# Kernel optimization log

Measured on AMD Instinct MI355X. Metric: run time of the kernel, lower is better.

Reference implementation:

```python
import jax, jax.numpy as jnp
import numpy as np

B, S, E, H = 4, 2048, 2048, 16
D = E // H  # head_dim = 128


def setup_inputs() -> dict:
    key = jax.random.key(0)
    kx, kq, kk, kv = jax.random.split(key, 4)
    std = 1.0 / np.sqrt(E)
    return {
        "x": jax.random.normal(kx, (B, S, E), dtype=jnp.float32),
        "Wq": jax.random.normal(kq, (E, E), dtype=jnp.float32) * std,
        "Wk": jax.random.normal(kk, (E, E), dtype=jnp.float32) * std,
        "Wv": jax.random.normal(kv, (E, E), dtype=jnp.float32) * std,
    }


def reference(x, Wq, Wk, Wv):
    b, s, _ = x.shape
    # nn.Linear(bias=False): y = x @ W.T
    q = (x @ Wq.T).reshape(b, s, H, D).transpose(0, 2, 1, 3)  # [b,h,s,d]
    k = (x @ Wk.T).reshape(b, s, H, D).transpose(0, 2, 1, 3)
    v = (x @ Wv.T).reshape(b, s, H, D).transpose(0, 2, 1, 3)
    scale = jnp.sqrt(jnp.asarray(D, dtype=jnp.float32))
    scores = jnp.einsum("bhqd,bhkd->bhqk", q, k) / scale  # [b,h,s,s]
    causal = jnp.tril(jnp.ones((s, s), dtype=bool))
    scores = jnp.where(causal, scores, -jnp.inf)
    weights = jax.nn.softmax(scores, axis=-1)
    attn = jnp.einsum("bhqk,bhkd->bhqd", weights, v)  # [b,h,s,d]
    return attn
```

## Files before the change

### kernel.cpp

```cpp
#include <hip/hip_runtime.h>
#include <hip/hip_bf16.h>
#include <stdint.h>

#define Bdim 4
#define Sdim 2048
#define Edim 2048
#define Hdim 16
#define Ddim 128

typedef unsigned short u16;
typedef unsigned int u32;
typedef __attribute__((ext_vector_type(8))) short bf16x8;
typedef __attribute__((ext_vector_type(4))) float f32x4;
typedef __attribute__((ext_vector_type(16))) float f32x16;
typedef __attribute__((ext_vector_type(4))) unsigned short u16x4;
typedef __attribute__((ext_vector_type(2))) unsigned int u32x2;

__device__ inline u16 f2bf(float f) {
  union { float f; uint32_t u; } v; v.f = f;
  uint32_t u = v.u;
  return (u16)((u + 0x7FFFu + ((u >> 16) & 1u)) >> 16);
}

__device__ inline u32 pkbf(float lo, float hi) {
  float2 t; t.x = lo; t.y = hi;
  union { __hip_bfloat162 h2; u32 u; } cv;
  cv.h2 = __float22bfloat162_rn(t);
  return cv.u;
}

__device__ inline f32x4 mfma16(bf16x8 a, bf16x8 b, f32x4 c) {
  return __builtin_amdgcn_mfma_f32_16x16x32_bf16(a, b, c, 0, 0, 0);
}
__device__ inline f32x16 mfma32(bf16x8 a, bf16x8 b, f32x16 c) {
  return __builtin_amdgcn_mfma_f32_32x32x16_bf16(a, b, c, 0, 0, 0);
}

__device__ inline void load_lds16(const void* g, const void* l) {
  __builtin_amdgcn_global_load_lds(
      (__attribute__((address_space(1))) void*)(uintptr_t)g,
      (__attribute__((address_space(3))) void*)(uint32_t)(uintptr_t)l,
      16, 0, 0);
}

__global__ void cvt_kernel(const float* __restrict__ src, u16* __restrict__ dst,
                           int n4, float scale) {
  int i = blockIdx.x * blockDim.x + threadIdx.x;
  if (i < n4) {
    float4 f = ((const float4*)src)[i];
    u16x4 o = { f2bf(f.x * scale), f2bf(f.y * scale),
                f2bf(f.z * scale), f2bf(f.w * scale) };
    ((u16x4*)dst)[i] = o;
  }
}

template <bool TRANSV>
__global__ __launch_bounds__(512, 2)
void gemm_nt(const u16* __restrict__ A, const u16* __restrict__ Bw,
             u16* __restrict__ C, int M, int N, int K) {
  __shared__ char lds[131072];

  const int tid = threadIdx.x;
  const int lane = tid & 63;
  const int w = tid >> 6;
  const int wm = w >> 2, wn = w & 3;
  const int bm = blockIdx.x, bn = blockIdx.y;
  const int NT = K >> 5;

  const int srow_off = lane >> 2;
  const int schunk = lane & 3;

  const int l15 = lane & 15;
  const int l4 = lane >> 4;
  const int rA = wm * 128 + l15;
  const int rB = wn * 64 + l15;
  const int gA = (rA + (rA >> 2)) & 3;
  const int gB = (rB + (rB >> 2)) & 3;
  const int aoff = rA * 64 + ((l4 ^ gA) << 4);
  const int boff = rB * 64 + ((l4 ^ gB) << 4);

  const u16* Agp = A + (size_t)(bm * 256) * K;
  const u16* Bgp = Bw + (size_t)(bn * 256) * K;

  f32x4 acc[8][4];
#pragma unroll
  for (int m = 0; m < 8; ++m)
#pragma unroll
    for (int n = 0; n < 4; ++n)
      acc[m][n] = (f32x4){0.f, 0.f, 0.f, 0.f};

#define GSTAGE(tt)                                                             \
  {                                                                            \
    const int slot_ = (tt) & 3;                                                \
    char* ab_ = lds + slot_ * 16384;                                           \
    char* bb_ = lds + 65536 + slot_ * 16384;                                   \
    _Pragma("unroll")                                                          \
    for (int i_ = 0; i_ < 2; ++i_) {                                           \
      const int rbase_ = w * 32 + i_ * 16;                                     \
      const int row_ = rbase_ + srow_off;                                      \
      const int src_ = schunk ^ ((row_ + (row_ >> 2)) & 3);                    \
      load_lds16(Agp + (size_t)row_ * K + (tt) * 32 + src_ * 8,                \
                 ab_ + rbase_ * 64);                                           \
      load_lds16(Bgp + (size_t)row_ * K + (tt) * 32 + src_ * 8,                \
                 bb_ + rbase_ * 64);                                           \
    }                                                                          \
  }

  GSTAGE(0);
  GSTAGE(1);
  asm volatile("s_waitcnt vmcnt(4)" ::: "memory");
  __builtin_amdgcn_s_barrier();

  for (int t = 0; t < NT; ++t) {
    if (t + 2 < NT) GSTAGE(t + 2);

    const char* ab = lds + (t & 3) * 16384 + aoff;
    const char* bb = lds + 65536 + (t & 3) * 16384 + boff;
    bf16x8 bfr[4];
#pragma unroll
    for (int n = 0; n < 4; ++n) bfr[n] = *(const bf16x8*)(bb + n * 1024);
    __builtin_amdgcn_s_setprio(1);
#pragma unroll
    for (int m = 0; m < 8; ++m) {
      bf16x8 af = *(const bf16x8*)(ab + m * 1024);
#pragma unroll
      for (int n = 0; n < 4; ++n) acc[m][n] = mfma16(af, bfr[n], acc[m][n]);
    }
    __builtin_amdgcn_s_setprio(0);

    if (t + 2 < NT) {
      asm volatile("s_waitcnt vmcnt(4)" ::: "memory");
      __builtin_amdgcn_s_barrier();
    } else if (t + 2 == NT) {
      asm volatile("s_waitcnt vmcnt(0)" ::: "memory");
      __builtin_amdgcn_s_barrier();
    }
  }
#undef GSTAGE

  const int r0 = bm * 256 + wm * 128 + (l4 << 2);
  const int c0 = bn * 256 + wn * 64 + l15;
  if (!TRANSV) {
#pragma unroll
    for (int m = 0; m < 8; ++m)
#pragma unroll
      for (int n = 0; n < 4; ++n) {
        int r = r0 + m * 16;
        int c = c0 + n * 16;
#pragma unroll
        for (int j = 0; j < 4; ++j)
          C[(size_t)(r + j) * N + c] = f2bf(acc[m][n][j]);
      }
  } else {
#pragma unroll
    for (int m = 0; m < 8; ++m)
#pragma unroll
      for (int n = 0; n < 4; ++n) {
        int ng = c0 + n * 16;
        int h = ng >> 7, d = ng & 127;
        int mg = r0 + m * 16;
        int b = mg >> 11, s = mg & 2047;
        u16x4 pk = { f2bf(acc[m][n][0]), f2bf(acc[m][n][1]),
                     f2bf(acc[m][n][2]), f2bf(acc[m][n][3]) };
        *(u16x4*)(C + ((size_t)((b * Hdim + h) * Ddim + d)) * Sdim + s) = pk;
      }
  }
}

__global__ __launch_bounds__(256)
void attn_kernel(const u16* __restrict__ Q, const u16* __restrict__ K,
                 const u16* __restrict__ Vt, float* __restrict__ O) {
  __shared__ u16 Ks[2][64 * 128];
  __shared__ u16 Vs[2][128 * 64];

  const int tid = threadIdx.x;
  const int lane = tid & 63;
  const int w = tid >> 6;
  const int l31 = lane & 31;
  const int hi = lane >> 5;

  const int bid = blockIdx.x;
  const int bh = bid & 63;
  const int qg = 15 - (bid >> 6);
  const int q0 = qg * 128;
  const int qw0 = q0 + w * 32;
  const int b = bh >> 4, h = bh & 15;

  const u16* Qb = Q + (size_t)b * Sdim * Edim + h * Ddim;
  const u16* Kb = K + (size_t)b * Sdim * Edim + h * Ddim;
  const u16* Vb = Vt + (size_t)bh * Ddim * Sdim;

  bf16x8 qf[8];
  {
    const u16* qrow = Qb + (size_t)(qw0 + l31) * Edim + hi * 8;
#pragma unroll
    for (int c = 0; c < 8; ++c) qf[c] = *(const bf16x8*)(qrow + c * 16);
  }

  f32x16 oacc[4];
#pragma unroll
  for (int d = 0; d < 4; ++d)
#pragma unroll
    for (int i = 0; i < 16; ++i) oacc[d][i] = 0.f;
  f32x16 lacc;
#pragma unroll
  for (int i = 0; i < 16; ++i) lacc[i] = 0.f;

  const short oneb = (short)0x3F80;
  const bf16x8 ones = {oneb, oneb, oneb, oneb, oneb, oneb, oneb, oneb};

  float m2 = -1e30f;
  const int qrel = qw0 + l31;

  const int nt = 2 * qg + 2;
  const int ntw = (qw0 + 31) / 64 + 1;

  const int krow_off = (lane >> 4);
  const int kchunk = lane & 15;
  const int vrow_off = (lane >> 3);
  const int vchunk = lane & 7;

#define STAGE(bufi, tt)                                                        \
  {                                                                            \
    const int kv0s = (tt) * 64;                                                \
    _Pragma("unroll")                                                          \
    for (int i = 0; i < 4; ++i) {                                              \
      const int rbase = w * 16 + i * 4;                                        \
      const int row = rbase + krow_off;                                        \
      const int cs = kchunk ^ (row & 15);                                      \
      load_lds16(Kb + (size_t)(kv0s + row) * Edim + cs * 8,                    \
                 &Ks[bufi][rbase * 128]);                                      \
    }                                                                          \
    _Pragma("unroll")                                                          \
    for (int i = 0; i < 4; ++i) {                                              \
      const int rbase = w * 32 + i * 8;                                        \
      const int row = rbase + vrow_off;                                        \
      const int cs = vchunk ^ (row & 7);                                       \
      load_lds16(Vb + (size_t)row * Sdim + kv0s + cs * 8,                      \
                 &Vs[bufi][rbase * 64]);                                       \
    }                                                                          \
  }

  STAGE(0, 0);
  __syncthreads();

  for (int t = 0; t < nt; ++t) {
    const int cur = t & 1;
    if (t + 1 < nt) STAGE(cur ^ 1, t + 1);

    if (t < ntw) {
      const int kv0 = t * 64;

      f32x16 sc0, sc1;
#pragma unroll
      for (int i = 0; i < 16; ++i) { sc0[i] = 0.f; sc1[i] = 0.f; }
#pragma unroll
      for (int c = 0; c < 8; ++c) {
        const int ch = c * 2 + hi;
        const int r0r = l31;
        const int r1r = 32 + l31;
        bf16x8 kf0 = *(const bf16x8*)&Ks[cur][r0r * 128 + (ch ^ (r0r & 15)) * 8];
        bf16x8 kf1 = *(const bf16x8*)&Ks[cur][r1r * 128 + (ch ^ (r1r & 15)) * 8];
        sc0 = mfma32(kf0, qf[c], sc0);
        sc1 = mfma32(kf1, qf[c], sc1);
      }

      float psc[32];
      float ma = -1e30f, mb = -1e30f, mc = -1e30f, md = -1e30f;
      if (kv0 + 64 > qw0) {
#pragma unroll
        for (int r = 0; r < 16; ++r) {
          const int cr = (r & 3) + 8 * (r >> 2) + 4 * hi;
          float v0 = (kv0 + cr <= qrel) ? sc0[r] : -1e30f;
          float v1 = (kv0 + 32 + cr <= qrel) ? sc1[r] : -1e30f;
          psc[r] = v0; psc[16 + r] = v1;
          if ((r & 3) == 0) { ma = fmaxf(fmaxf(ma, v0), v1); }
          else if ((r & 3) == 1) { mb = fmaxf(fmaxf(mb, v0), v1); }
          else if ((r & 3) == 2) { mc = fmaxf(fmaxf(mc, v0), v1); }
          else { md = fmaxf(fmaxf(md, v0), v1); }
        }
      } else {
#pragma unroll
        for (int r = 0; r < 16; ++r) {
          float v0 = sc0[r];
          float v1 = sc1[r];
          psc[r] = v0; psc[16 + r] = v1;
          if ((r & 3) == 0) { ma = fmaxf(fmaxf(ma, v0), v1); }
          else if ((r & 3) == 1) { mb = fmaxf(fmaxf(mb, v0), v1); }
          else if ((r & 3) == 2) { mc = fmaxf(fmaxf(mc, v0), v1); }
          else { md = fmaxf(fmaxf(md, v0), v1); }
        }
      }
      float mt = fmaxf(fmaxf(ma, mb), fmaxf(mc, md));
      u32x2 mx = __builtin_amdgcn_permlane32_swap(
          __float_as_uint(mt), __float_as_uint(mt), false, false);
      float mo = fmaxf(__uint_as_float(mx.x), __uint_as_float(mx.y));

      if (__any(mo - m2 > 8.0f)) {
        float mnew = fmaxf(m2, mo);
        float corr = __builtin_amdgcn_exp2f(m2 - mnew);
        m2 = mnew;
        lacc[0] *= corr;
#pragma unroll
        for (int d = 0; d < 4; ++d)
#pragma unroll
          for (int i = 0; i < 16; ++i) oacc[d][i] *= corr;
      }

#pragma unroll
      for (int r = 0; r < 32; ++r)
        psc[r] = __builtin_amdgcn_exp2f(psc[r] - m2);

      u32 pk[16];
#pragma unroll
      for (int i = 0; i < 16; ++i) pk[i] = pkbf(psc[2 * i], psc[2 * i + 1]);
      bf16x8 pa[4];
#pragma unroll
      for (int t2 = 0; t2 < 2; ++t2)
#pragma unroll
        for (int q2 = 0; q2 < 2; ++q2) {
          const int base = t2 * 8 + q2 * 4;
          u32x2 r0 = __builtin_amdgcn_permlane32_swap(pk[base + 0], pk[base + 2],
                                                      false, false);
          u32x2 r1 = __builtin_amdgcn_permlane32_swap(pk[base + 1], pk[base + 3],
                                                      false, false);
          union { u32 wv[4]; bf16x8 v; } cv;
          cv.wv[0] = r0.x; cv.wv[1] = r1.x; cv.wv[2] = r0.y; cv.wv[3] = r1.y;
          pa[t2 * 2 + q2] = cv.v;
        }

#pragma unroll
      for (int dblk = 0; dblk < 4; ++dblk) {
        const int row = dblk * 32 + l31;
#pragma unroll
        for (int ks = 0; ks < 4; ++ks) {
          const int ch = ks * 2 + hi;
          bf16x8 vf = *(const bf16x8*)&Vs[cur][row * 64 + (ch ^ (row & 7)) * 8];
          oacc[dblk] = mfma32(vf, pa[ks], oacc[dblk]);
        }
      }
#pragma unroll
      for (int ks = 0; ks < 4; ++ks) lacc = mfma32(ones, pa[ks], lacc);
    }

    __syncthreads();
  }

  float inv = 1.0f / lacc[0];
  float* Ob = O + ((size_t)bh * Sdim + qw0 + l31) * Ddim + hi * 4;
#pragma unroll
  for (int dblk = 0; dblk < 4; ++dblk)
#pragma unroll
    for (int g = 0; g < 4; ++g) {
      f32x4 o4 = { oacc[dblk][4 * g] * inv, oacc[dblk][4 * g + 1] * inv,
                   oacc[dblk][4 * g + 2] * inv, oacc[dblk][4 * g + 3] * inv };
      *(f32x4*)(Ob + dblk * 32 + g * 8) = o4;
    }
}

extern "C" void kernel_launch(void* const* d_in, const int* in_sizes, int n_in,
                              void* d_out, int out_size, void* d_ws, size_t ws_size,
                              hipStream_t stream) {
  const float* x  = (const float*)d_in[0];
  const float* Wq = (const float*)d_in[1];
  const float* Wk = (const float*)d_in[2];
  const float* Wv = (const float*)d_in[3];
  float* out = (float*)d_out;
  char* ws = (char*)d_ws;

  u16* xb  = (u16*)(ws);
  u16* wqb = (u16*)(ws + 33554432ull);
  u16* wkb = (u16*)(ws + 41943040ull);
  u16* wvb = (u16*)(ws + 50331648ull);
  u16* Qb  = (u16*)(ws + 58720256ull);
  u16* Kb  = (u16*)(ws + 92274688ull);
  u16* Vt  = (u16*)(ws + 125829120ull);

  const int nX = Bdim * Sdim * Edim;
  const int nW = Edim * Edim;
  const float K1SC = 0.08838834764831845f * 1.4426950408889634f;
  cvt_kernel<<<(nX / 4 + 255) / 256, 256, 0, stream>>>(x, xb, nX / 4, 1.0f);
  cvt_kernel<<<(nW / 4 + 255) / 256, 256, 0, stream>>>(Wq, wqb, nW / 4, K1SC);
  cvt_kernel<<<(nW / 4 + 255) / 256, 256, 0, stream>>>(Wk, wkb, nW / 4, 1.0f);
  cvt_kernel<<<(nW / 4 + 255) / 256, 256, 0, stream>>>(Wv, wvb, nW / 4, 1.0f);

  dim3 g(Bdim * Sdim / 256, Edim / 256);
  gemm_nt<false><<<g, 512, 0, stream>>>(xb, wqb, Qb, Bdim * Sdim, Edim, Edim);
  gemm_nt<false><<<g, 512, 0, stream>>>(xb, wkb, Kb, Bdim * Sdim, Edim, Edim);
  gemm_nt<true ><<<g, 512, 0, stream>>>(xb, wvb, Vt, Bdim * Sdim, Edim, Edim);

  attn_kernel<<<Bdim * Hdim * (Sdim / 128), 256, 0, stream>>>(Qb, Kb, Vt, out);
}
```

Measured before the change: 374.3 us.

## Fuse QKV GEMMs into one launch and deepen attention KV pipeline with smaller tiles

The three weight conversions are merged into one kernel, and the three projection GEMMs become a single launch with a z-dimension that selects weight and output. The attention kernel moves from 64-key tiles with double buffering to 32-key tiles in a 4-slot ring with two tiles in flight. It replaces __syncthreads with explicit vmcnt waits and adds s_setprio around the MFMA sections. The diagonal mask now applies to only one 32-wide tile per wave, which trims wasted masked work. The cost is twice as many loop iterations and barriers per query block, and a reworked V swizzle that may change LDS bank behaviour.

Result: slower. 407.2 us (+8.8%).

```diff
diff --git a/kernel.cpp b/kernel.cpp
--- a/kernel.cpp
+++ b/kernel.cpp
@@ -54,11 +54,30 @@
   }
 }
 
-template <bool TRANSV>
+__global__ void cvt_w_kernel(const float* __restrict__ Wq,
+                             const float* __restrict__ Wk,
+                             const float* __restrict__ Wv,
+                             u16* __restrict__ dst, float qscale) {
+  int i = blockIdx.x * blockDim.x + threadIdx.x;
+  int seg = i >> 20;
+  int off = i & 1048575;
+  const float* src = seg == 0 ? Wq : (seg == 1 ? Wk : Wv);
+  float sc = seg == 0 ? qscale : 1.0f;
+  float4 f = ((const float4*)src)[off];
+  u16x4 o = { f2bf(f.x * sc), f2bf(f.y * sc), f2bf(f.z * sc), f2bf(f.w * sc) };
+  ((u16x4*)dst)[i] = o;
+}
+
 __global__ __launch_bounds__(512, 2)
-void gemm_nt(const u16* __restrict__ A, const u16* __restrict__ Bw,
-             u16* __restrict__ C, int M, int N, int K) {
+void gemm_qkv(const u16* __restrict__ A, const u16* __restrict__ W0,
+              const u16* __restrict__ W1, const u16* __restrict__ W2,
+              u16* __restrict__ C0, u16* __restrict__ C1, u16* __restrict__ C2,
+              int M, int N, int K) {
   __shared__ char lds[131072];
+
+  const int z = blockIdx.z;
+  const u16* Bw = z == 0 ? W0 : (z == 1 ? W1 : W2);
+  u16* C = z == 0 ? C0 : (z == 1 ? C1 : C2);
 
   const int tid = threadIdx.x;
   const int lane = tid & 63;
@@ -140,7 +159,7 @@
 
   const int r0 = bm * 256 + wm * 128 + (l4 << 2);
   const int c0 = bn * 256 + wn * 64 + l15;
-  if (!TRANSV) {
+  if (z < 2) {
 #pragma unroll
     for (int m = 0; m < 8; ++m)
 #pragma unroll
@@ -170,8 +189,8 @@
 __global__ __launch_bounds__(256)
 void attn_kernel(const u16* __restrict__ Q, const u16* __restrict__ K,
                  const u16* __restrict__ Vt, float* __restrict__ O) {
-  __shared__ u16 Ks[2][64 * 128];
-  __shared__ u16 Vs[2][128 * 64];
+  __shared__ u16 Ks[4][32 * 128];
+  __shared__ u16 Vs[4][128 * 32];
 
   const int tid = threadIdx.x;
   const int lane = tid & 63;
@@ -210,85 +229,83 @@
   const bf16x8 ones = {oneb, oneb, oneb, oneb, oneb, oneb, oneb, oneb};
 
   float m2 = -1e30f;
-  const int qrel = qw0 + l31;
-
-  const int nt = 2 * qg + 2;
-  const int ntw = (qw0 + 31) / 64 + 1;
-
-  const int krow_off = (lane >> 4);
+
+  const int nt = 4 * qg + 4;
+  const int tdiag = qw0 >> 5;
+  const int ntw = tdiag + 1;
+
+  const int krow_off = lane >> 4;
   const int kchunk = lane & 15;
-  const int vrow_off = (lane >> 3);
-  const int vchunk = lane & 7;
-
-#define STAGE(bufi, tt)                                                        \
+  const int vrow_off = lane >> 2;
+  const int vchunk = lane & 3;
+
+#define STAGE(tt)                                                              \
   {                                                                            \
-    const int kv0s = (tt) * 64;                                                \
+    const int slot_ = (tt) & 3;                                                \
+    const int kv0s = (tt) * 32;                                                \
     _Pragma("unroll")                                                          \
-    for (int i = 0; i < 4; ++i) {                                              \
-      const int rbase = w * 16 + i * 4;                                        \
+    for (int i = 0; i < 2; ++i) {                                              \
+      const int rbase = w * 8 + i * 4;                                         \
       const int row = rbase + krow_off;                                        \
       const int cs = kchunk ^ (row & 15);                                      \
       load_lds16(Kb + (size_t)(kv0s + row) * Edim + cs * 8,                    \
-                 &Ks[bufi][rbase * 128]);                                      \
+                 &Ks[slot_][rbase * 128]);                                     \
     }                                                                          \
     _Pragma("unroll")                                                          \
-    for (int i = 0; i < 4; ++i) {                                              \
-      const int rbase = w * 32 + i * 8;                                        \
+    for (int i = 0; i < 2; ++i) {                                              \
+      const int rbase = w * 32 + i * 16;                                       \
       const int row = rbase + vrow_off;                                        \
-      const int cs = vchunk ^ (row & 7);                                       \
+      const int cs = vchunk ^ ((row >> 1) & 3);                                \
       load_lds16(Vb + (size_t)row * Sdim + kv0s + cs * 8,                      \
-                 &Vs[bufi][rbase * 64]);                                       \
+                 &Vs[slot_][rbase * 32]);                                      \
     }                                                                          \
   }
 
-  STAGE(0, 0);
-  __syncthreads();
+  STAGE(0);
+  STAGE(1);
+  asm volatile("s_waitcnt vmcnt(4)" ::: "memory");
+  __builtin_amdgcn_s_barrier();
 
   for (int t = 0; t < nt; ++t) {
-    const int cur = t & 1;
-    if (t + 1 < nt) STAGE(cur ^ 1, t + 1);
+    if (t + 2 < nt) STAGE(t + 2);
 
     if (t < ntw) {
-      const int kv0 = t * 64;
-
-      f32x16 sc0, sc1;
-#pragma unroll
-      for (int i = 0; i < 16; ++i) { sc0[i] = 0.f; sc1[i] = 0.f; }
+      const int cur = t & 3;
+
+      f32x16 sc;
+#pragma unroll
+      for (int i = 0; i < 16; ++i) sc[i] = 0.f;
+      __builtin_amdgcn_s_setprio(1);
 #pragma unroll
       for (int c = 0; c < 8; ++c) {
         const int ch = c * 2 + hi;
-        const int r0r = l31;
-        const int r1r = 32 + l31;
-        bf16x8 kf0 = *(const bf16x8*)&Ks[cur][r0r * 128 + (ch ^ (r0r & 15)) * 8];
-        bf16x8 kf1 = *(const bf16x8*)&Ks[cur][r1r * 128 + (ch ^ (r1r & 15)) * 8];
-        sc0 = mfma32(kf0, qf[c], sc0);
-        sc1 = mfma32(kf1, qf[c], sc1);
-      }
-
-      float psc[32];
+        bf16x8 kf = *(const bf16x8*)&Ks[cur][l31 * 128 + ((ch ^ (l31 & 15)) * 8)];
+        sc = mfma32(kf, qf[c], sc);
+      }
+      __builtin_amdgcn_s_setprio(0);
+
+      float psc[16];
       float ma = -1e30f, mb = -1e30f, mc = -1e30f, md = -1e30f;
-      if (kv0 + 64 > qw0) {
+      if (t == tdiag) {
 #pragma unroll
         for (int r = 0; r < 16; ++r) {
           const int cr = (r & 3) + 8 * (r >> 2) + 4 * hi;
-          float v0 = (kv0 + cr <= qrel) ? sc0[r] : -1e30f;
-          float v1 = (kv0 + 32 + cr <= qrel) ? sc1[r] : -1e30f;
-          psc[r] = v0; psc[16 + r] = v1;
-          if ((r & 3) == 0) { ma = fmaxf(fmaxf(ma, v0), v1); }
-          else if ((r & 3) == 1) { mb = fmaxf(fmaxf(mb, v0), v1); }
-          else if ((r & 3) == 2) { mc = fmaxf(fmaxf(mc, v0), v1); }
-          else { md = fmaxf(fmaxf(md, v0), v1); }
+          float v = (cr <= l31) ? sc[r] : -1e30f;
+          psc[r] = v;
+          if ((r & 3) == 0) ma = fmaxf(ma, v);
+          else if ((r & 3) == 1) mb = fmaxf(mb, v);
+          else if ((r & 3) == 2) mc = fmaxf(mc, v);
+          else md = fmaxf(md, v);
         }
       } else {
 #pragma unroll
         for (int r = 0; r < 16; ++r) {
-          float v0 = sc0[r];
-          float v1 = sc1[r];
-          psc[r] = v0; psc[16 + r] = v1;
-          if ((r & 3) == 0) { ma = fmaxf(fmaxf(ma, v0), v1); }
-          else if ((r & 3) == 1) { mb = fmaxf(fmaxf(mb, v0), v1); }
-          else if ((r & 3) == 2) { mc = fmaxf(fmaxf(mc, v0), v1); }
-          else { md = fmaxf(fmaxf(md, v0), v1); }
+          float v = sc[r];
+          psc[r] = v;
+          if ((r & 3) == 0) ma = fmaxf(ma, v);
+          else if ((r & 3) == 1) mb = fmaxf(mb, v);
+          else if ((r & 3) == 2) mc = fmaxf(mc, v);
+          else md = fmaxf(md, v);
         }
       }
       float mt = fmaxf(fmaxf(ma, mb), fmaxf(mc, md));
@@ -308,43 +325,50 @@
       }
 
 #pragma unroll
-      for (int r = 0; r < 32; ++r)
+      for (int r = 0; r < 16; ++r)
         psc[r] = __builtin_amdgcn_exp2f(psc[r] - m2);
 
-      u32 pk[16];
-#pragma unroll
-      for (int i = 0; i < 16; ++i) pk[i] = pkbf(psc[2 * i], psc[2 * i + 1]);
-      bf16x8 pa[4];
-#pragma unroll
-      for (int t2 = 0; t2 < 2; ++t2)
-#pragma unroll
-        for (int q2 = 0; q2 < 2; ++q2) {
-          const int base = t2 * 8 + q2 * 4;
-          u32x2 r0 = __builtin_amdgcn_permlane32_swap(pk[base + 0], pk[base + 2],
-                                                      false, false);
-          u32x2 r1 = __builtin_amdgcn_permlane32_swap(pk[base + 1], pk[base + 3],
-                                                      false, false);
-          union { u32 wv[4]; bf16x8 v; } cv;
-          cv.wv[0] = r0.x; cv.wv[1] = r1.x; cv.wv[2] = r0.y; cv.wv[3] = r1.y;
-          pa[t2 * 2 + q2] = cv.v;
-        }
-
+      u32 pk[8];
+#pragma unroll
+      for (int i = 0; i < 8; ++i) pk[i] = pkbf(psc[2 * i], psc[2 * i + 1]);
+      bf16x8 pa[2];
+#pragma unroll
+      for (int q2 = 0; q2 < 2; ++q2) {
+        const int base = q2 * 4;
+        u32x2 r0 = __builtin_amdgcn_permlane32_swap(pk[base + 0], pk[base + 2],
+                                                    false, false);
+        u32x2 r1 = __builtin_amdgcn_permlane32_swap(pk[base + 1], pk[base + 3],
+                                                    false, false);
+        union { u32 wv[4]; bf16x8 v; } cv;
+        cv.wv[0] = r0.x; cv.wv[1] = r1.x; cv.wv[2] = r0.y; cv.wv[3] = r1.y;
+        pa[q2] = cv.v;
+      }
+
+      __builtin_amdgcn_s_setprio(1);
 #pragma unroll
       for (int dblk = 0; dblk < 4; ++dblk) {
         const int row = dblk * 32 + l31;
 #pragma unroll
-        for (int ks = 0; ks < 4; ++ks) {
+        for (int ks = 0; ks < 2; ++ks) {
           const int ch = ks * 2 + hi;
-          bf16x8 vf = *(const bf16x8*)&Vs[cur][row * 64 + (ch ^ (row & 7)) * 8];
+          bf16x8 vf = *(const bf16x8*)&Vs[cur][row * 32 + ((ch ^ ((row >> 1) & 3)) * 8)];
           oacc[dblk] = mfma32(vf, pa[ks], oacc[dblk]);
         }
       }
 #pragma unroll
-      for (int ks = 0; ks < 4; ++ks) lacc = mfma32(ones, pa[ks], lacc);
+      for (int ks = 0; ks < 2; ++ks) lacc = mfma32(ones, pa[ks], lacc);
+      __builtin_amdgcn_s_setprio(0);
     }
 
-    __syncthreads();
-  }
+    if (t + 2 < nt) {
+      asm volatile("s_waitcnt vmcnt(4)" ::: "memory");
+      __builtin_amdgcn_s_barrier();
+    } else {
+      asm volatile("s_waitcnt vmcnt(0)" ::: "memory");
+      __builtin_amdgcn_s_barrier();
+    }
+  }
+#undef STAGE
 
   float inv = 1.0f / lacc[0];
   float* Ob = O + ((size_t)bh * Sdim + qw0 + l31) * Ddim + hi * 4;
@@ -380,14 +404,11 @@
   const int nW = Edim * Edim;
   const float K1SC = 0.08838834764831845f * 1.4426950408889634f;
   cvt_kernel<<<(nX / 4 + 255) / 256, 256, 0, stream>>>(x, xb, nX / 4, 1.0f);
-  cvt_kernel<<<(nW / 4 + 255) / 256, 256, 0, stream>>>(Wq, wqb, nW / 4, K1SC);
-  cvt_kernel<<<(nW / 4 + 255) / 256, 256, 0, stream>>>(Wk, wkb, nW / 4, 1.0f);
-  cvt_kernel<<<(nW / 4 + 255) / 256, 256, 0, stream>>>(Wv, wvb, nW / 4, 1.0f);
-
-  dim3 g(Bdim * Sdim / 256, Edim / 256);
-  gemm_nt<false><<<g, 512, 0, stream>>>(xb, wqb, Qb, Bdim * Sdim, Edim, Edim);
-  gemm_nt<false><<<g, 512, 0, stream>>>(xb, wkb, Kb, Bdim * Sdim, Edim, Edim);
-  gemm_nt<true ><<<g, 512, 0, stream>>>(xb, wvb, Vt, Bdim * Sdim, Edim, Edim);
+  cvt_w_kernel<<<(3 * nW / 4 + 255) / 256, 256, 0, stream>>>(Wq, Wk, Wv, wqb, K1SC);
+
+  dim3 g(Bdim * Sdim / 256, Edim / 256, 3);
+  gemm_qkv<<<g, 512, 0, stream>>>(xb, wqb, wkb, wvb, Qb, Kb, Vt,
+                                  Bdim * Sdim, Edim, Edim);
 
   attn_kernel<<<Bdim * Hdim * (Sdim / 128), 256, 0, stream>>>(Qb, Kb, Vt, out);
 }
```

## Interleave GEMM prefetch with split MFMA phases, add setprio in attention, fuse weight casts

Applied to the files above, without the earlier changes.

The GEMM main loop now runs in two halves. It prefetches the A tile before the first half of the MFMAs and the B tile before the second half, with extra barriers between the phases, so global-to-LDS loads spread out across compute. The attention kernel raises wave priority around its MFMA blocks. The three weight-conversion launches are merged into one kernel that writes the contiguous wq/wk/wv buffers. The extra barriers per iteration add synchronisation cost in exchange for better overlap.

After: 388.4 us. 1.04x slower.

```diff
diff --git a/kernel.cpp b/kernel.cpp
--- a/kernel.cpp
+++ b/kernel.cpp
@@ -54,6 +54,20 @@
   }
 }
 
+__global__ void cvt_w_kernel(const float* __restrict__ Wq,
+                             const float* __restrict__ Wk,
+                             const float* __restrict__ Wv,
+                             u16* __restrict__ dst, float qscale) {
+  int i = blockIdx.x * blockDim.x + threadIdx.x;
+  int seg = i >> 20;
+  int off = i & 1048575;
+  const float* src = seg == 0 ? Wq : (seg == 1 ? Wk : Wv);
+  float sc = seg == 0 ? qscale : 1.0f;
+  float4 f = ((const float4*)src)[off];
+  u16x4 o = { f2bf(f.x * sc), f2bf(f.y * sc), f2bf(f.z * sc), f2bf(f.w * sc) };
+  ((u16x4*)dst)[i] = o;
+}
+
 template <bool TRANSV>
 __global__ __launch_bounds__(512, 2)
 void gemm_nt(const u16* __restrict__ A, const u16* __restrict__ Bw,
@@ -89,11 +103,9 @@
     for (int n = 0; n < 4; ++n)
       acc[m][n] = (f32x4){0.f, 0.f, 0.f, 0.f};
 
-#define GSTAGE(tt)                                                             \
+#define GSTAGE_A(tt)                                                           \
   {                                                                            \
-    const int slot_ = (tt) & 3;                                                \
-    char* ab_ = lds + slot_ * 16384;                                           \
-    char* bb_ = lds + 65536 + slot_ * 16384;                                   \
+    char* ab_ = lds + ((tt) & 3) * 16384;                                      \
     _Pragma("unroll")                                                          \
     for (int i_ = 0; i_ < 2; ++i_) {                                           \
       const int rbase_ = w * 32 + i_ * 16;                                     \
@@ -101,42 +113,66 @@
       const int src_ = schunk ^ ((row_ + (row_ >> 2)) & 3);                    \
       load_lds16(Agp + (size_t)row_ * K + (tt) * 32 + src_ * 8,                \
                  ab_ + rbase_ * 64);                                           \
+    }                                                                          \
+  }
+#define GSTAGE_B(tt)                                                           \
+  {                                                                            \
+    char* bb_ = lds + 65536 + ((tt) & 3) * 16384;                              \
+    _Pragma("unroll")                                                          \
+    for (int i_ = 0; i_ < 2; ++i_) {                                           \
+      const int rbase_ = w * 32 + i_ * 16;                                     \
+      const int row_ = rbase_ + srow_off;                                      \
+      const int src_ = schunk ^ ((row_ + (row_ >> 2)) & 3);                    \
       load_lds16(Bgp + (size_t)row_ * K + (tt) * 32 + src_ * 8,                \
                  bb_ + rbase_ * 64);                                           \
     }                                                                          \
   }
 
-  GSTAGE(0);
-  GSTAGE(1);
+  GSTAGE_A(0); GSTAGE_B(0);
+  GSTAGE_A(1); GSTAGE_B(1);
   asm volatile("s_waitcnt vmcnt(4)" ::: "memory");
   __builtin_amdgcn_s_barrier();
 
   for (int t = 0; t < NT; ++t) {
-    if (t + 2 < NT) GSTAGE(t + 2);
-
     const char* ab = lds + (t & 3) * 16384 + aoff;
     const char* bb = lds + 65536 + (t & 3) * 16384 + boff;
-    bf16x8 bfr[4];
+    const bool pf = (t + 2 < NT);
+
+    bf16x8 bfr[4], afr[4];
 #pragma unroll
     for (int n = 0; n < 4; ++n) bfr[n] = *(const bf16x8*)(bb + n * 1024);
+#pragma unroll
+    for (int m = 0; m < 4; ++m) afr[m] = *(const bf16x8*)(ab + m * 1024);
+    if (pf) GSTAGE_A(t + 2);
+    __builtin_amdgcn_s_barrier();
     __builtin_amdgcn_s_setprio(1);
 #pragma unroll
-    for (int m = 0; m < 8; ++m) {
-      bf16x8 af = *(const bf16x8*)(ab + m * 1024);
-#pragma unroll
-      for (int n = 0; n < 4; ++n) acc[m][n] = mfma16(af, bfr[n], acc[m][n]);
+    for (int m = 0; m < 4; ++m)
+#pragma unroll
+      for (int n = 0; n < 4; ++n) acc[m][n] = mfma16(afr[m], bfr[n], acc[m][n]);
+    __builtin_amdgcn_s_setprio(0);
+    __builtin_amdgcn_s_barrier();
+
+#pragma unroll
+    for (int m = 0; m < 4; ++m) afr[m] = *(const bf16x8*)(ab + (m + 4) * 1024);
+    if (pf) GSTAGE_B(t + 2);
+    __builtin_amdgcn_s_barrier();
+    __builtin_amdgcn_s_setprio(1);
+#pragma unroll
+    for (int m = 0; m < 4; ++m)
+#pragma unroll
+      for (int n = 0; n < 4; ++n)
+        acc[m + 4][n] = mfma16(afr[m], bfr[n], acc[m + 4][n]);
+    __builtin_amdgcn_s_setprio(0);
+    if (pf) {
+      asm volatile("s_waitcnt vmcnt(4)" ::: "memory");
+    } else {
+      asm volatile("s_waitcnt vmcnt(0)" ::: "memory");
     }
-    __builtin_amdgcn_s_setprio(0);
-
-    if (t + 2 < NT) {
-      asm volatile("s_waitcnt vmcnt(4)" ::: "memory");
-      __builtin_amdgcn_s_barrier();
-    } else if (t + 2 == NT) {
-      asm volatile("s_waitcnt vmcnt(0)" ::: "memory");
-      __builtin_amdgcn_s_barrier();
-    }
-  }
-#undef GSTAGE
+    __builtin_amdgcn_s_barrier();
+  }
+#undef GSTAGE_A
+#undef GSTAGE_B
 
   const int r0 = bm * 256 + wm * 128 + (l4 << 2);
   const int c0 = bn * 256 + wn * 64 + l15;
@@ -254,6 +290,7 @@
       f32x16 sc0, sc1;
 #pragma unroll
       for (int i = 0; i < 16; ++i) { sc0[i] = 0.f; sc1[i] = 0.f; }
+      __builtin_amdgcn_s_setprio(1);
 #pragma unroll
       for (int c = 0; c < 8; ++c) {
         const int ch = c * 2 + hi;
@@ -264,6 +301,7 @@
         sc0 = mfma32(kf0, qf[c], sc0);
         sc1 = mfma32(kf1, qf[c], sc1);
       }
+      __builtin_amdgcn_s_setprio(0);
 
       float psc[32];
       float ma = -1e30f, mb = -1e30f, mc = -1e30f, md = -1e30f;
@@ -329,6 +367,7 @@
           pa[t2 * 2 + q2] = cv.v;
         }
 
+      __builtin_amdgcn_s_setprio(1);
 #pragma unroll
       for (int dblk = 0; dblk < 4; ++dblk) {
         const int row = dblk * 32 + l31;
@@ -341,10 +380,12 @@
       }
 #pragma unroll
       for (int ks = 0; ks < 4; ++ks) lacc = mfma32(ones, pa[ks], lacc);
+      __builtin_amdgcn_s_setprio(0);
     }
 
     __syncthreads();
   }
+#undef STAGE
 
   float inv = 1.0f / lacc[0];
   float* Ob = O + ((size_t)bh * Sdim + qw0 + l31) * Ddim + hi * 4;
@@ -380,9 +421,7 @@
   const int nW = Edim * Edim;
   const float K1SC = 0.08838834764831845f * 1.4426950408889634f;
   cvt_kernel<<<(nX / 4 + 255) / 256, 256, 0, stream>>>(x, xb, nX / 4, 1.0f);
-  cvt_kernel<<<(nW / 4 + 255) / 256, 256, 0, stream>>>(Wq, wqb, nW / 4, K1SC);
-  cvt_kernel<<<(nW / 4 + 255) / 256, 256, 0, stream>>>(Wk, wkb, nW / 4, 1.0f);
-  cvt_kernel<<<(nW / 4 + 255) / 256, 256, 0, stream>>>(Wv, wvb, nW / 4, 1.0f);
+  cvt_w_kernel<<<(3 * nW / 4 + 255) / 256, 256, 0, stream>>>(Wq, Wk, Wv, wqb, K1SC);
 
   dim3 g(Bdim * Sdim / 256, Edim / 256);
   gemm_nt<false><<<g, 512, 0, stream>>>(xb, wqb, Qb, Bdim * Sdim, Edim, Edim);
```

## Read V fragments directly from global memory and merge weight conversions

Applied to the files above, without the earlier changes.

The attention kernel no longer stages V tiles into LDS. Each lane reads its bf16x8 V fragments straight from global memory (which L2 should cache) just before the PV MFMAs, which halves the LDS footprint and removes the V async copies. The three weight-conversion launches are also merged into one kernel, relying on the contiguous wqb/wkb/wvb workspace layout. The risk is that the global loads sit on the MFMA critical path with no prefetch, so their latency may stall the PV stage.

Measured after the change: 492.5 us. 31.6% more time.

```diff
diff --git a/kernel.cpp b/kernel.cpp
--- a/kernel.cpp
+++ b/kernel.cpp
@@ -52,6 +52,20 @@
                 f2bf(f.z * scale), f2bf(f.w * scale) };
     ((u16x4*)dst)[i] = o;
   }
+}
+
+__global__ void cvt_w_kernel(const float* __restrict__ Wq,
+                             const float* __restrict__ Wk,
+                             const float* __restrict__ Wv,
+                             u16* __restrict__ dst, float qscale) {
+  int i = blockIdx.x * blockDim.x + threadIdx.x;
+  int seg = i >> 20;
+  int off = i & 1048575;
+  const float* src = seg == 0 ? Wq : (seg == 1 ? Wk : Wv);
+  float sc = seg == 0 ? qscale : 1.0f;
+  float4 f = ((const float4*)src)[off];
+  u16x4 o = { f2bf(f.x * sc), f2bf(f.y * sc), f2bf(f.z * sc), f2bf(f.w * sc) };
+  ((u16x4*)dst)[i] = o;
 }
 
 template <bool TRANSV>
@@ -171,7 +185,6 @@
 void attn_kernel(const u16* __restrict__ Q, const u16* __restrict__ K,
                  const u16* __restrict__ Vt, float* __restrict__ O) {
   __shared__ u16 Ks[2][64 * 128];
-  __shared__ u16 Vs[2][128 * 64];
 
   const int tid = threadIdx.x;
   const int lane = tid & 63;
@@ -217,8 +230,8 @@
 
   const int krow_off = (lane >> 4);
   const int kchunk = lane & 15;
-  const int vrow_off = (lane >> 3);
-  const int vchunk = lane & 7;
+
+  const u16* vbase = Vb + (size_t)l31 * Sdim + hi * 8;
 
 #define STAGE(bufi, tt)                                                        \
   {                                                                            \
@@ -231,14 +244,6 @@
       load_lds16(Kb + (size_t)(kv0s + row) * Edim + cs * 8,                    \
                  &Ks[bufi][rbase * 128]);                                      \
     }                                                                          \
-    _Pragma("unroll")                                                          \
-    for (int i = 0; i < 4; ++i) {                                              \
-      const int rbase = w * 32 + i * 8;                                        \
-      const int row = rbase + vrow_off;                                        \
-      const int cs = vchunk ^ (row & 7);                                       \
-      load_lds16(Vb + (size_t)row * Sdim + kv0s + cs * 8,                      \
-                 &Vs[bufi][rbase * 64]);                                       \
-    }                                                                          \
   }
 
   STAGE(0, 0);
@@ -331,11 +336,10 @@
 
 #pragma unroll
       for (int dblk = 0; dblk < 4; ++dblk) {
-        const int row = dblk * 32 + l31;
+        const u16* vrow = vbase + (size_t)(dblk * 32) * Sdim + kv0;
 #pragma unroll
         for (int ks = 0; ks < 4; ++ks) {
-          const int ch = ks * 2 + hi;
-          bf16x8 vf = *(const bf16x8*)&Vs[cur][row * 64 + (ch ^ (row & 7)) * 8];
+          bf16x8 vf = *(const bf16x8*)(vrow + ks * 16);
           oacc[dblk] = mfma32(vf, pa[ks], oacc[dblk]);
         }
       }
@@ -345,6 +349,7 @@
 
     __syncthreads();
   }
+#undef STAGE
 
   float inv = 1.0f / lacc[0];
   float* Ob = O + ((size_t)bh * Sdim + qw0 + l31) * Ddim + hi * 4;
@@ -380,9 +385,7 @@
   const int nW = Edim * Edim;
   const float K1SC = 0.08838834764831845f * 1.4426950408889634f;
   cvt_kernel<<<(nX / 4 + 255) / 256, 256, 0, stream>>>(x, xb, nX / 4, 1.0f);
-  cvt_kernel<<<(nW / 4 + 255) / 256, 256, 0, stream>>>(Wq, wqb, nW / 4, K1SC);
-  cvt_kernel<<<(nW / 4 + 255) / 256, 256, 0, stream>>>(Wk, wkb, nW / 4, 1.0f);
-  cvt_kernel<<<(nW / 4 + 255) / 256, 256, 0, stream>>>(Wv, wvb, nW / 4, 1.0f);
+  cvt_w_kernel<<<(3 * nW / 4 + 255) / 256, 256, 0, stream>>>(Wq, Wk, Wv, wqb, K1SC);
 
   dim3 g(Bdim * Sdim / 256, Edim / 256);
   gemm_nt<false><<<g, 512, 0, stream>>>(xb, wqb, Qb, Bdim * Sdim, Edim, Edim);
```
